# Kernel tuning notes

Measured on AMD Instinct MI355X. Metric: run time of the kernel, lower is better.

The kernel has to match this reference:

```python
import jax, jax.numpy as jnp
import numpy as np

S, B, H, I, E = 512, 2, 1024, 2816, 8  # seq_len, batch, hidden, intermediate, num_local_experts


def setup_inputs() -> dict:
    key = jax.random.key(0)
    ks = jax.random.split(key, 5)
    return {
        "hidden_states": jax.random.normal(ks[0], (S, B, H), dtype=jnp.float32),
        "router_w": jax.random.normal(ks[1], (E, H), dtype=jnp.float32) * 0.02,
        "gate_w": jax.random.normal(ks[2], (E, I, H), dtype=jnp.float32) * 0.02,
        "up_w": jax.random.normal(ks[3], (E, I, H), dtype=jnp.float32) * 0.02,
        "down_w": jax.random.normal(ks[4], (E, H, I), dtype=jnp.float32) * 0.02,
    }


def reference(hidden_states, router_w, gate_w, up_w, down_w):
    # Router: linear hidden -> num_experts, top-1 routing (num_experts_per_tok == 1).
    router_logits = jnp.einsum('sbh,eh->sbe', hidden_states, router_w)  # [S,B,E]
    routing_indices = jnp.argmax(router_logits, axis=-1)  # [S,B], top-1 == argmax
    # NOTE: the source computes routing_weights = sigmoid(top logit) but never
    # applies it in _combine_expert_outputs; we faithfully omit the scaling.

    out = jnp.zeros_like(hidden_states)
    for e in range(E):  # fixed small expert count; masked dense dispatch/combine
        mask = (routing_indices == e)[..., None]  # [S,B,1]
        xe = jnp.where(mask, hidden_states, 0.0)
        g = jnp.einsum('sbh,ih->sbi', xe, gate_w[e])
        u = jnp.einsum('sbh,ih->sbi', xe, up_w[e])
        ye = jnp.einsum('sbi,hi->sbh', jax.nn.silu(g) * u, down_w[e])
        out = out + jnp.where(mask, ye, 0.0)
    return out
```

## Files before the change

### kernel.cpp

```cpp
#include <hip/hip_runtime.h>
#include <math.h>

constexpr int H_ = 1024;
constexpr int I_ = 2816;
constexpr int E_ = 8;
constexpr int T_ = 1024;

typedef __bf16 bf16x8 __attribute__((ext_vector_type(8)));
typedef float f32x4 __attribute__((ext_vector_type(4)));

__device__ __forceinline__ ushort f2bf(float f) {
    uint32_t u = __float_as_uint(f);
    u += 0x7fff + ((u >> 16) & 1);
    return (ushort)(u >> 16);
}
__device__ __forceinline__ uint pack2(float lo, float hi) {
    return (uint)f2bf(lo) | ((uint)f2bf(hi) << 16);
}


__global__ __launch_bounds__(64) void init_counts_kernel(int* __restrict__ counts) {
    if (threadIdx.x < E_) counts[threadIdx.x] = 0;
}

__global__ __launch_bounds__(64) void router_kernel(const float* __restrict__ hidden,
                                                    const float* __restrict__ rw,
                                                    int* __restrict__ counts,
                                                    int* __restrict__ tlist) {
    const int t = blockIdx.x;
    const int lane = threadIdx.x;
    const float* x = hidden + (size_t)t * H_;
    float acc[E_];
#pragma unroll
    for (int e = 0; e < E_; e++) acc[e] = 0.f;
    for (int h = lane; h < H_; h += 64) {
        float xv = x[h];
#pragma unroll
        for (int e = 0; e < E_; e++) acc[e] = fmaf(xv, rw[e * H_ + h], acc[e]);
    }
#pragma unroll
    for (int e = 0; e < E_; e++) {
#pragma unroll
        for (int off = 32; off >= 1; off >>= 1)
            acc[e] += __shfl_xor(acc[e], off, 64);
    }
    if (lane == 0) {
        int best = 0;
        float bv = acc[0];
#pragma unroll
        for (int e = 1; e < E_; e++) {
            if (acc[e] > bv) { bv = acc[e]; best = e; }
        }
        int pos = atomicAdd(&counts[best], 1);
        tlist[best * T_ + pos] = t;
    }
}

__global__ __launch_bounds__(256) void gateup_kernel(const float* __restrict__ hidden,
                                                     const float* __restrict__ gate_w,
                                                     const float* __restrict__ up_w,
                                                     const int* __restrict__ counts,
                                                     const int* __restrict__ tlist,
                                                     ushort* __restrict__ act) {
    const int e  = blockIdx.y >> 3;
    const int tt = blockIdx.y & 7;
    const int cnt = counts[e];
    if (tt * 128 >= cnt) return;
    const int i0 = blockIdx.x * 64;
    const int tid = threadIdx.x;

    __shared__ ushort Xs[128 * 72];
    __shared__ ushort Gs[64 * 72];
    __shared__ ushort Us[64 * 72];
    __shared__ int toks[128];

    if (tid < 128) {
        int p = tt * 128 + tid;
        toks[tid] = (p < cnt) ? tlist[e * T_ + p] : -1;
    }
    __syncthreads();

    const float* gw = gate_w + (size_t)e * I_ * H_ + (size_t)i0 * H_;
    const float* uw = up_w   + (size_t)e * I_ * H_ + (size_t)i0 * H_;

    f32x4 accg[8], accu[8];
#pragma unroll
    for (int mi = 0; mi < 8; mi++) {
        accg[mi] = (f32x4){0.f, 0.f, 0.f, 0.f};
        accu[mi] = (f32x4){0.f, 0.f, 0.f, 0.f};
    }

    const int wv = tid >> 6;
    const int lane = tid & 63;
    const int quad = lane >> 4;
    const int l15 = lane & 15;

    for (int k0 = 0; k0 < H_; k0 += 64) {
        float4 xv[8];
#pragma unroll
        for (int p = 0; p < 8; p++) {
            int idx = tid + p * 256;
            int row = idx >> 4, c4 = (idx & 15) << 2;
            int tok = toks[row];
            xv[p] = (tok >= 0) ? *(const float4*)(hidden + (size_t)tok * H_ + k0 + c4)
                               : make_float4(0.f, 0.f, 0.f, 0.f);
        }
        float4 gv[4], uv[4];
#pragma unroll
        for (int p = 0; p < 4; p++) {
            int idx = tid + p * 256;
            int row = idx >> 4, c4 = (idx & 15) << 2;
            gv[p] = *(const float4*)(gw + (size_t)row * H_ + k0 + c4);
            uv[p] = *(const float4*)(uw + (size_t)row * H_ + k0 + c4);
        }
        __syncthreads();
#pragma unroll
        for (int p = 0; p < 8; p++) {
            int idx = tid + p * 256;
            int row = idx >> 4, c4 = (idx & 15) << 2;
            *(uint2*)&Xs[row * 72 + c4] = (uint2){pack2(xv[p].x, xv[p].y), pack2(xv[p].z, xv[p].w)};
        }
#pragma unroll
        for (int p = 0; p < 4; p++) {
            int idx = tid + p * 256;
            int row = idx >> 4, c4 = (idx & 15) << 2;
            *(uint2*)&Gs[row * 72 + c4] = (uint2){pack2(gv[p].x, gv[p].y), pack2(gv[p].z, gv[p].w)};
            *(uint2*)&Us[row * 72 + c4] = (uint2){pack2(uv[p].x, uv[p].y), pack2(uv[p].z, uv[p].w)};
        }
        __syncthreads();
#pragma unroll
        for (int kk = 0; kk < 64; kk += 32) {
            const int kb = kk + quad * 8;
            bf16x8 bg = *(const bf16x8*)&Gs[(wv * 16 + l15) * 72 + kb];
            bf16x8 bu = *(const bf16x8*)&Us[(wv * 16 + l15) * 72 + kb];
#pragma unroll
            for (int mi = 0; mi < 8; mi++) {
                bf16x8 a = *(const bf16x8*)&Xs[(mi * 16 + l15) * 72 + kb];
                accg[mi] = __builtin_amdgcn_mfma_f32_16x16x32_bf16(a, bg, accg[mi], 0, 0, 0);
                accu[mi] = __builtin_amdgcn_mfma_f32_16x16x32_bf16(a, bu, accu[mi], 0, 0, 0);
            }
        }
        __syncthreads();
    }

#pragma unroll
    for (int mi = 0; mi < 8; mi++) {
#pragma unroll
        for (int r = 0; r < 4; r++) {
            int tok = toks[mi * 16 + quad * 4 + r];
            if (tok < 0) continue;
            float g = accg[mi][r], u = accu[mi][r];
            float s = g / (1.f + __expf(-g)) * u;
            act[(size_t)tok * I_ + i0 + wv * 16 + l15] = f2bf(s);
        }
    }
}

__global__ __launch_bounds__(256) void down_kernel(const ushort* __restrict__ act,
                                                   const float* __restrict__ down_w,
                                                   const int* __restrict__ counts,
                                                   const int* __restrict__ tlist,
                                                   float* __restrict__ out) {
    const int e  = blockIdx.y >> 3;
    const int tt = blockIdx.y & 7;
    const int cnt = counts[e];
    if (tt * 128 >= cnt) return;
    const int h0 = blockIdx.x * 32;
    const int tid = threadIdx.x;

    __shared__ ushort As[128 * 72];
    __shared__ ushort Ds[32 * 72];
    __shared__ int toks[128];

    if (tid < 128) {
        int p = tt * 128 + tid;
        toks[tid] = (p < cnt) ? tlist[e * T_ + p] : -1;
    }
    __syncthreads();

    const float* dw = down_w + (size_t)e * H_ * I_ + (size_t)h0 * I_;

    f32x4 acc[2][2];
#pragma unroll
    for (int mi = 0; mi < 2; mi++)
#pragma unroll
        for (int nj = 0; nj < 2; nj++) acc[mi][nj] = (f32x4){0.f, 0.f, 0.f, 0.f};

    const int wv = tid >> 6;
    const int lane = tid & 63;
    const int quad = lane >> 4;
    const int l15 = lane & 15;

    for (int k0 = 0; k0 < I_; k0 += 64) {
        uint4 av[4];
#pragma unroll
        for (int p = 0; p < 4; p++) {
            int idx = tid + p * 256;
            int row = idx >> 3, c8 = (idx & 7) << 3;
            int tok = toks[row];
            av[p] = (tok >= 0) ? *(const uint4*)(act + (size_t)tok * I_ + k0 + c8)
                               : (uint4){0u, 0u, 0u, 0u};
        }
        float4 dv[2];
#pragma unroll
        for (int p = 0; p < 2; p++) {
            int idx = tid + p * 256;
            int row = idx >> 4, c4 = (idx & 15) << 2;
            dv[p] = *(const float4*)(dw + (size_t)row * I_ + k0 + c4);
        }
        __syncthreads();
#pragma unroll
        for (int p = 0; p < 4; p++) {
            int idx = tid + p * 256;
            int row = idx >> 3, c8 = (idx & 7) << 3;
            *(uint4*)&As[row * 72 + c8] = av[p];
        }
#pragma unroll
        for (int p = 0; p < 2; p++) {
            int idx = tid + p * 256;
            int row = idx >> 4, c4 = (idx & 15) << 2;
            *(uint2*)&Ds[row * 72 + c4] = (uint2){pack2(dv[p].x, dv[p].y), pack2(dv[p].z, dv[p].w)};
        }
        __syncthreads();
#pragma unroll
        for (int kk = 0; kk < 64; kk += 32) {
            const int kb = kk + quad * 8;
            bf16x8 a0 = *(const bf16x8*)&As[(wv * 32 +      l15) * 72 + kb];
            bf16x8 a1 = *(const bf16x8*)&As[(wv * 32 + 16 + l15) * 72 + kb];
            bf16x8 b0 = *(const bf16x8*)&Ds[(     l15) * 72 + kb];
            bf16x8 b1 = *(const bf16x8*)&Ds[(16 + l15) * 72 + kb];
            acc[0][0] = __builtin_amdgcn_mfma_f32_16x16x32_bf16(a0, b0, acc[0][0], 0, 0, 0);
            acc[0][1] = __builtin_amdgcn_mfma_f32_16x16x32_bf16(a0, b1, acc[0][1], 0, 0, 0);
            acc[1][0] = __builtin_amdgcn_mfma_f32_16x16x32_bf16(a1, b0, acc[1][0], 0, 0, 0);
            acc[1][1] = __builtin_amdgcn_mfma_f32_16x16x32_bf16(a1, b1, acc[1][1], 0, 0, 0);
        }
        __syncthreads();
    }

#pragma unroll
    for (int mi = 0; mi < 2; mi++) {
#pragma unroll
        for (int r = 0; r < 4; r++) {
            int tok = toks[wv * 32 + mi * 16 + quad * 4 + r];
            if (tok < 0) continue;
#pragma unroll
            for (int nj = 0; nj < 2; nj++)
                out[(size_t)tok * H_ + h0 + nj * 16 + l15] = acc[mi][nj][r];
        }
    }
}

extern "C" void kernel_launch(void* const* d_in, const int* in_sizes, int n_in,
                              void* d_out, int out_size, void* d_ws, size_t ws_size,
                              hipStream_t stream) {
    const float* hidden = (const float*)d_in[0];
    const float* rw     = (const float*)d_in[1];
    const float* gate_w = (const float*)d_in[2];
    const float* up_w   = (const float*)d_in[3];
    const float* down_w = (const float*)d_in[4];
    float* out = (float*)d_out;

    int* counts = (int*)d_ws;
    int* tlist  = counts + E_;
    ushort* act = (ushort*)(tlist + E_ * T_);

    hipLaunchKernelGGL(init_counts_kernel, dim3(1), dim3(64), 0, stream, counts);
    hipLaunchKernelGGL(router_kernel, dim3(T_), dim3(64), 0, stream, hidden, rw, counts, tlist);
    hipLaunchKernelGGL(gateup_kernel, dim3(I_ / 64, E_ * 8), dim3(256), 0, stream,
                       hidden, gate_w, up_w, counts, tlist, act);
    hipLaunchKernelGGL(down_kernel, dim3(H_ / 32, E_ * 8), dim3(256), 0, stream,
                       act, down_w, counts, tlist, out);
}
```

Before: 441.2 us.

## Stream expert weights once per block with token-loop tiles and register prefetch

The router now also writes a bf16 copy of the hidden states, so later stages gather half the bytes and skip repeated conversion. The gate/up and down kernels launch one block per (column tile, expert) and loop over that expert's tokens in chunks of 256. Each weight tile is therefore read once per expert instead of once per 128-token tile, and the next K-slice is prefetched into registers while the current one is used. This cuts the grid to fewer blocks (I/32 x 8 and H/32 x 8), which risks lower occupancy and load imbalance when experts get uneven token counts.

```diff
diff --git a/kernel.cpp b/kernel.cpp
--- a/kernel.cpp
+++ b/kernel.cpp
@@ -19,24 +19,31 @@
 }
 
 
-__global__ __launch_bounds__(64) void init_counts_kernel(int* __restrict__ counts) {
-    if (threadIdx.x < E_) counts[threadIdx.x] = 0;
-}
-
 __global__ __launch_bounds__(64) void router_kernel(const float* __restrict__ hidden,
                                                     const float* __restrict__ rw,
                                                     int* __restrict__ counts,
-                                                    int* __restrict__ tlist) {
+                                                    int* __restrict__ tlist,
+                                                    ushort* __restrict__ xbf) {
     const int t = blockIdx.x;
     const int lane = threadIdx.x;
-    const float* x = hidden + (size_t)t * H_;
+    const float* x = hidden + (size_t)t * H_ + lane * 16;
+    float4 v[4];
+#pragma unroll
+    for (int j = 0; j < 4; j++) v[j] = ((const float4*)x)[j];
+    uint2* xb = (uint2*)(xbf + (size_t)t * H_ + lane * 16);
+#pragma unroll
+    for (int j = 0; j < 4; j++) xb[j] = make_uint2(pack2(v[j].x, v[j].y), pack2(v[j].z, v[j].w));
     float acc[E_];
 #pragma unroll
-    for (int e = 0; e < E_; e++) acc[e] = 0.f;
-    for (int h = lane; h < H_; h += 64) {
-        float xv = x[h];
-#pragma unroll
-        for (int e = 0; e < E_; e++) acc[e] = fmaf(xv, rw[e * H_ + h], acc[e]);
+    for (int e = 0; e < E_; e++) {
+        const float4* r = (const float4*)(rw + e * H_ + lane * 16);
+        float a = 0.f;
+#pragma unroll
+        for (int j = 0; j < 4; j++) {
+            float4 rv = r[j];
+            a += v[j].x * rv.x + v[j].y * rv.y + v[j].z * rv.z + v[j].w * rv.w;
+        }
+        acc[e] = a;
     }
 #pragma unroll
     for (int e = 0; e < E_; e++) {
@@ -56,197 +63,241 @@
     }
 }
 
-__global__ __launch_bounds__(256) void gateup_kernel(const float* __restrict__ hidden,
-                                                     const float* __restrict__ gate_w,
-                                                     const float* __restrict__ up_w,
-                                                     const int* __restrict__ counts,
-                                                     const int* __restrict__ tlist,
-                                                     ushort* __restrict__ act) {
-    const int e  = blockIdx.y >> 3;
-    const int tt = blockIdx.y & 7;
+__global__ __launch_bounds__(256, 3) void gateup_kernel(const ushort* __restrict__ xbf,
+                                                        const float* __restrict__ gate_w,
+                                                        const float* __restrict__ up_w,
+                                                        const int* __restrict__ counts,
+                                                        const int* __restrict__ tlist,
+                                                        ushort* __restrict__ act) {
+    const int e  = blockIdx.y;
+    const int i0 = blockIdx.x * 32;
     const int cnt = counts[e];
-    if (tt * 128 >= cnt) return;
-    const int i0 = blockIdx.x * 64;
     const int tid = threadIdx.x;
 
-    __shared__ ushort Xs[128 * 72];
-    __shared__ ushort Gs[64 * 72];
-    __shared__ ushort Us[64 * 72];
-    __shared__ int toks[128];
-
-    if (tid < 128) {
-        int p = tt * 128 + tid;
-        toks[tid] = (p < cnt) ? tlist[e * T_ + p] : -1;
-    }
-    __syncthreads();
-
+    __shared__ ushort Xs[256 * 72];
+    __shared__ ushort Gs[32 * 72];
+    __shared__ ushort Us[32 * 72];
+    __shared__ int toks[256];
+
+    const int wv = tid >> 6, lane = tid & 63, quad = lane >> 4, l15 = lane & 15;
     const float* gw = gate_w + (size_t)e * I_ * H_ + (size_t)i0 * H_;
     const float* uw = up_w   + (size_t)e * I_ * H_ + (size_t)i0 * H_;
 
-    f32x4 accg[8], accu[8];
-#pragma unroll
-    for (int mi = 0; mi < 8; mi++) {
-        accg[mi] = (f32x4){0.f, 0.f, 0.f, 0.f};
-        accu[mi] = (f32x4){0.f, 0.f, 0.f, 0.f};
-    }
-
-    const int wv = tid >> 6;
-    const int lane = tid & 63;
-    const int quad = lane >> 4;
-    const int l15 = lane & 15;
-
-    for (int k0 = 0; k0 < H_; k0 += 64) {
-        float4 xv[8];
+    for (int toff = 0; toff < cnt; toff += 256) {
+        __syncthreads();
+        {
+            int p = toff + tid;
+            toks[tid] = (p < cnt) ? tlist[e * T_ + p] : -1;
+        }
+        __syncthreads();
+        int tokr[8];
+#pragma unroll
+        for (int p = 0; p < 8; p++) tokr[p] = toks[(tid + p * 256) >> 3];
+
+        f32x4 accg[4][2], accu[4][2];
+#pragma unroll
+        for (int mi = 0; mi < 4; mi++)
+#pragma unroll
+            for (int nj = 0; nj < 2; nj++) {
+                accg[mi][nj] = (f32x4){0.f, 0.f, 0.f, 0.f};
+                accu[mi][nj] = (f32x4){0.f, 0.f, 0.f, 0.f};
+            }
+
+        uint4 xv[8];
+        float4 gv[2], uv[2];
 #pragma unroll
         for (int p = 0; p < 8; p++) {
             int idx = tid + p * 256;
-            int row = idx >> 4, c4 = (idx & 15) << 2;
-            int tok = toks[row];
-            xv[p] = (tok >= 0) ? *(const float4*)(hidden + (size_t)tok * H_ + k0 + c4)
-                               : make_float4(0.f, 0.f, 0.f, 0.f);
-        }
-        float4 gv[4], uv[4];
-#pragma unroll
-        for (int p = 0; p < 4; p++) {
-            int idx = tid + p * 256;
-            int row = idx >> 4, c4 = (idx & 15) << 2;
-            gv[p] = *(const float4*)(gw + (size_t)row * H_ + k0 + c4);
-            uv[p] = *(const float4*)(uw + (size_t)row * H_ + k0 + c4);
-        }
-        __syncthreads();
-#pragma unroll
-        for (int p = 0; p < 8; p++) {
-            int idx = tid + p * 256;
-            int row = idx >> 4, c4 = (idx & 15) << 2;
-            *(uint2*)&Xs[row * 72 + c4] = (uint2){pack2(xv[p].x, xv[p].y), pack2(xv[p].z, xv[p].w)};
-        }
-#pragma unroll
-        for (int p = 0; p < 4; p++) {
-            int idx = tid + p * 256;
-            int row = idx >> 4, c4 = (idx & 15) << 2;
-            *(uint2*)&Gs[row * 72 + c4] = (uint2){pack2(gv[p].x, gv[p].y), pack2(gv[p].z, gv[p].w)};
-            *(uint2*)&Us[row * 72 + c4] = (uint2){pack2(uv[p].x, uv[p].y), pack2(uv[p].z, uv[p].w)};
-        }
-        __syncthreads();
-#pragma unroll
-        for (int kk = 0; kk < 64; kk += 32) {
-            const int kb = kk + quad * 8;
-            bf16x8 bg = *(const bf16x8*)&Gs[(wv * 16 + l15) * 72 + kb];
-            bf16x8 bu = *(const bf16x8*)&Us[(wv * 16 + l15) * 72 + kb];
-#pragma unroll
-            for (int mi = 0; mi < 8; mi++) {
-                bf16x8 a = *(const bf16x8*)&Xs[(mi * 16 + l15) * 72 + kb];
-                accg[mi] = __builtin_amdgcn_mfma_f32_16x16x32_bf16(a, bg, accg[mi], 0, 0, 0);
-                accu[mi] = __builtin_amdgcn_mfma_f32_16x16x32_bf16(a, bu, accu[mi], 0, 0, 0);
-            }
-        }
-        __syncthreads();
-    }
-
-#pragma unroll
-    for (int mi = 0; mi < 8; mi++) {
-#pragma unroll
-        for (int r = 0; r < 4; r++) {
-            int tok = toks[mi * 16 + quad * 4 + r];
-            if (tok < 0) continue;
-            float g = accg[mi][r], u = accu[mi][r];
-            float s = g / (1.f + __expf(-g)) * u;
-            act[(size_t)tok * I_ + i0 + wv * 16 + l15] = f2bf(s);
-        }
-    }
-}
-
-__global__ __launch_bounds__(256) void down_kernel(const ushort* __restrict__ act,
-                                                   const float* __restrict__ down_w,
-                                                   const int* __restrict__ counts,
-                                                   const int* __restrict__ tlist,
-                                                   float* __restrict__ out) {
-    const int e  = blockIdx.y >> 3;
-    const int tt = blockIdx.y & 7;
-    const int cnt = counts[e];
-    if (tt * 128 >= cnt) return;
-    const int h0 = blockIdx.x * 32;
-    const int tid = threadIdx.x;
-
-    __shared__ ushort As[128 * 72];
-    __shared__ ushort Ds[32 * 72];
-    __shared__ int toks[128];
-
-    if (tid < 128) {
-        int p = tt * 128 + tid;
-        toks[tid] = (p < cnt) ? tlist[e * T_ + p] : -1;
-    }
-    __syncthreads();
-
-    const float* dw = down_w + (size_t)e * H_ * I_ + (size_t)h0 * I_;
-
-    f32x4 acc[2][2];
-#pragma unroll
-    for (int mi = 0; mi < 2; mi++)
-#pragma unroll
-        for (int nj = 0; nj < 2; nj++) acc[mi][nj] = (f32x4){0.f, 0.f, 0.f, 0.f};
-
-    const int wv = tid >> 6;
-    const int lane = tid & 63;
-    const int quad = lane >> 4;
-    const int l15 = lane & 15;
-
-    for (int k0 = 0; k0 < I_; k0 += 64) {
-        uint4 av[4];
-#pragma unroll
-        for (int p = 0; p < 4; p++) {
-            int idx = tid + p * 256;
-            int row = idx >> 3, c8 = (idx & 7) << 3;
-            int tok = toks[row];
-            av[p] = (tok >= 0) ? *(const uint4*)(act + (size_t)tok * I_ + k0 + c8)
-                               : (uint4){0u, 0u, 0u, 0u};
-        }
-        float4 dv[2];
+            xv[p] = (tokr[p] >= 0)
+                ? *(const uint4*)(xbf + (size_t)tokr[p] * H_ + ((idx & 7) << 3))
+                : make_uint4(0u, 0u, 0u, 0u);
+        }
 #pragma unroll
         for (int p = 0; p < 2; p++) {
             int idx = tid + p * 256;
             int row = idx >> 4, c4 = (idx & 15) << 2;
-            dv[p] = *(const float4*)(dw + (size_t)row * I_ + k0 + c4);
-        }
+            gv[p] = *(const float4*)(gw + (size_t)row * H_ + c4);
+            uv[p] = *(const float4*)(uw + (size_t)row * H_ + c4);
+        }
+
+        for (int k0 = 0; k0 < H_; k0 += 64) {
+            __syncthreads();
+#pragma unroll
+            for (int p = 0; p < 8; p++) {
+                int idx = tid + p * 256;
+                *(uint4*)&Xs[(idx >> 3) * 72 + ((idx & 7) << 3)] = xv[p];
+            }
+#pragma unroll
+            for (int p = 0; p < 2; p++) {
+                int idx = tid + p * 256;
+                int row = idx >> 4, c4 = (idx & 15) << 2;
+                *(uint2*)&Gs[row * 72 + c4] = make_uint2(pack2(gv[p].x, gv[p].y), pack2(gv[p].z, gv[p].w));
+                *(uint2*)&Us[row * 72 + c4] = make_uint2(pack2(uv[p].x, uv[p].y), pack2(uv[p].z, uv[p].w));
+            }
+            if (k0 + 64 < H_) {
+                int kn = k0 + 64;
+#pragma unroll
+                for (int p = 0; p < 8; p++) {
+                    int idx = tid + p * 256;
+                    xv[p] = (tokr[p] >= 0)
+                        ? *(const uint4*)(xbf + (size_t)tokr[p] * H_ + kn + ((idx & 7) << 3))
+                        : make_uint4(0u, 0u, 0u, 0u);
+                }
+#pragma unroll
+                for (int p = 0; p < 2; p++) {
+                    int idx = tid + p * 256;
+                    int row = idx >> 4, c4 = (idx & 15) << 2;
+                    gv[p] = *(const float4*)(gw + (size_t)row * H_ + kn + c4);
+                    uv[p] = *(const float4*)(uw + (size_t)row * H_ + kn + c4);
+                }
+            }
+            __syncthreads();
+#pragma unroll
+            for (int kk = 0; kk < 64; kk += 32) {
+                const int kb = kk + quad * 8;
+                bf16x8 bg[2], bu[2], a[4];
+#pragma unroll
+                for (int nj = 0; nj < 2; nj++) {
+                    bg[nj] = *(const bf16x8*)&Gs[(nj * 16 + l15) * 72 + kb];
+                    bu[nj] = *(const bf16x8*)&Us[(nj * 16 + l15) * 72 + kb];
+                }
+#pragma unroll
+                for (int mi = 0; mi < 4; mi++)
+                    a[mi] = *(const bf16x8*)&Xs[(wv * 64 + mi * 16 + l15) * 72 + kb];
+#pragma unroll
+                for (int mi = 0; mi < 4; mi++)
+#pragma unroll
+                    for (int nj = 0; nj < 2; nj++) {
+                        accg[mi][nj] = __builtin_amdgcn_mfma_f32_16x16x32_bf16(a[mi], bg[nj], accg[mi][nj], 0, 0, 0);
+                        accu[mi][nj] = __builtin_amdgcn_mfma_f32_16x16x32_bf16(a[mi], bu[nj], accu[mi][nj], 0, 0, 0);
+                    }
+            }
+        }
+
+#pragma unroll
+        for (int mi = 0; mi < 4; mi++)
+#pragma unroll
+            for (int r = 0; r < 4; r++) {
+                int tok = toks[wv * 64 + mi * 16 + quad * 4 + r];
+                if (tok < 0) continue;
+#pragma unroll
+                for (int nj = 0; nj < 2; nj++) {
+                    float g = accg[mi][nj][r], u = accu[mi][nj][r];
+                    float s = g / (1.f + __expf(-g)) * u;
+                    act[(size_t)tok * I_ + i0 + nj * 16 + l15] = f2bf(s);
+                }
+            }
+    }
+}
+
+__global__ __launch_bounds__(256, 3) void down_kernel(const ushort* __restrict__ act,
+                                                      const float* __restrict__ down_w,
+                                                      const int* __restrict__ counts,
+                                                      const int* __restrict__ tlist,
+                                                      float* __restrict__ out) {
+    const int e  = blockIdx.y;
+    const int h0 = blockIdx.x * 32;
+    const int cnt = counts[e];
+    const int tid = threadIdx.x;
+
+    __shared__ ushort As[256 * 72];
+    __shared__ ushort Ds[32 * 72];
+    __shared__ int toks[256];
+
+    const int wv = tid >> 6, lane = tid & 63, quad = lane >> 4, l15 = lane & 15;
+    const float* dw = down_w + (size_t)e * H_ * I_ + (size_t)h0 * I_;
+
+    for (int toff = 0; toff < cnt; toff += 256) {
         __syncthreads();
-#pragma unroll
-        for (int p = 0; p < 4; p++) {
+        {
+            int p = toff + tid;
+            toks[tid] = (p < cnt) ? tlist[e * T_ + p] : -1;
+        }
+        __syncthreads();
+        int tokr[8];
+#pragma unroll
+        for (int p = 0; p < 8; p++) tokr[p] = toks[(tid + p * 256) >> 3];
+
+        f32x4 acc[4][2];
+#pragma unroll
+        for (int mi = 0; mi < 4; mi++)
+#pragma unroll
+            for (int nj = 0; nj < 2; nj++) acc[mi][nj] = (f32x4){0.f, 0.f, 0.f, 0.f};
+
+        uint4 av[8];
+        float4 dv[2];
+#pragma unroll
+        for (int p = 0; p < 8; p++) {
             int idx = tid + p * 256;
-            int row = idx >> 3, c8 = (idx & 7) << 3;
-            *(uint4*)&As[row * 72 + c8] = av[p];
+            av[p] = (tokr[p] >= 0)
+                ? *(const uint4*)(act + (size_t)tokr[p] * I_ + ((idx & 7) << 3))
+                : make_uint4(0u, 0u, 0u, 0u);
         }
 #pragma unroll
         for (int p = 0; p < 2; p++) {
             int idx = tid + p * 256;
             int row = idx >> 4, c4 = (idx & 15) << 2;
-            *(uint2*)&Ds[row * 72 + c4] = (uint2){pack2(dv[p].x, dv[p].y), pack2(dv[p].z, dv[p].w)};
-        }
-        __syncthreads();
-#pragma unroll
-        for (int kk = 0; kk < 64; kk += 32) {
-            const int kb = kk + quad * 8;
-            bf16x8 a0 = *(const bf16x8*)&As[(wv * 32 +      l15) * 72 + kb];
-            bf16x8 a1 = *(const bf16x8*)&As[(wv * 32 + 16 + l15) * 72 + kb];
-            bf16x8 b0 = *(const bf16x8*)&Ds[(     l15) * 72 + kb];
-            bf16x8 b1 = *(const bf16x8*)&Ds[(16 + l15) * 72 + kb];
-            acc[0][0] = __builtin_amdgcn_mfma_f32_16x16x32_bf16(a0, b0, acc[0][0], 0, 0, 0);
-            acc[0][1] = __builtin_amdgcn_mfma_f32_16x16x32_bf16(a0, b1, acc[0][1], 0, 0, 0);
-            acc[1][0] = __builtin_amdgcn_mfma_f32_16x16x32_bf16(a1, b0, acc[1][0], 0, 0, 0);
-            acc[1][1] = __builtin_amdgcn_mfma_f32_16x16x32_bf16(a1, b1, acc[1][1], 0, 0, 0);
-        }
-        __syncthreads();
-    }
-
-#pragma unroll
-    for (int mi = 0; mi < 2; mi++) {
-#pragma unroll
-        for (int r = 0; r < 4; r++) {
-            int tok = toks[wv * 32 + mi * 16 + quad * 4 + r];
-            if (tok < 0) continue;
-#pragma unroll
-            for (int nj = 0; nj < 2; nj++)
-                out[(size_t)tok * H_ + h0 + nj * 16 + l15] = acc[mi][nj][r];
-        }
+            dv[p] = *(const float4*)(dw + (size_t)row * I_ + c4);
+        }
+
+        for (int k0 = 0; k0 < I_; k0 += 64) {
+            __syncthreads();
+#pragma unroll
+            for (int p = 0; p < 8; p++) {
+                int idx = tid + p * 256;
+                *(uint4*)&As[(idx >> 3) * 72 + ((idx & 7) << 3)] = av[p];
+            }
+#pragma unroll
+            for (int p = 0; p < 2; p++) {
+                int idx = tid + p * 256;
+                int row = idx >> 4, c4 = (idx & 15) << 2;
+                *(uint2*)&Ds[row * 72 + c4] = make_uint2(pack2(dv[p].x, dv[p].y), pack2(dv[p].z, dv[p].w));
+            }
+            if (k0 + 64 < I_) {
+                int kn = k0 + 64;
+#pragma unroll
+                for (int p = 0; p < 8; p++) {
+                    int idx = tid + p * 256;
+                    av[p] = (tokr[p] >= 0)
+                        ? *(const uint4*)(act + (size_t)tokr[p] * I_ + kn + ((idx & 7) << 3))
+                        : make_uint4(0u, 0u, 0u, 0u);
+                }
+#pragma unroll
+                for (int p = 0; p < 2; p++) {
+                    int idx = tid + p * 256;
+                    int row = idx >> 4, c4 = (idx & 15) << 2;
+                    dv[p] = *(const float4*)(dw + (size_t)row * I_ + kn + c4);
+                }
+            }
+            __syncthreads();
+#pragma unroll
+            for (int kk = 0; kk < 64; kk += 32) {
+                const int kb = kk + quad * 8;
+                bf16x8 b[2], a[4];
+#pragma unroll
+                for (int nj = 0; nj < 2; nj++)
+                    b[nj] = *(const bf16x8*)&Ds[(nj * 16 + l15) * 72 + kb];
+#pragma unroll
+                for (int mi = 0; mi < 4; mi++)
+                    a[mi] = *(const bf16x8*)&As[(wv * 64 + mi * 16 + l15) * 72 + kb];
+#pragma unroll
+                for (int mi = 0; mi < 4; mi++)
+#pragma unroll
+                    for (int nj = 0; nj < 2; nj++)
+                        acc[mi][nj] = __builtin_amdgcn_mfma_f32_16x16x32_bf16(a[mi], b[nj], acc[mi][nj], 0, 0, 0);
+            }
+        }
+
+#pragma unroll
+        for (int mi = 0; mi < 4; mi++)
+#pragma unroll
+            for (int r = 0; r < 4; r++) {
+                int tok = toks[wv * 64 + mi * 16 + quad * 4 + r];
+                if (tok < 0) continue;
+#pragma unroll
+                for (int nj = 0; nj < 2; nj++)
+                    out[(size_t)tok * H_ + h0 + nj * 16 + l15] = acc[mi][nj][r];
+            }
     }
 }
 
@@ -262,12 +313,13 @@
 
     int* counts = (int*)d_ws;
     int* tlist  = counts + E_;
-    ushort* act = (ushort*)(tlist + E_ * T_);
-
-    hipLaunchKernelGGL(init_counts_kernel, dim3(1), dim3(64), 0, stream, counts);
-    hipLaunchKernelGGL(router_kernel, dim3(T_), dim3(64), 0, stream, hidden, rw, counts, tlist);
-    hipLaunchKernelGGL(gateup_kernel, dim3(I_ / 64, E_ * 8), dim3(256), 0, stream,
-                       hidden, gate_w, up_w, counts, tlist, act);
-    hipLaunchKernelGGL(down_kernel, dim3(H_ / 32, E_ * 8), dim3(256), 0, stream,
+    ushort* xbf = (ushort*)(tlist + E_ * T_);
+    ushort* act = xbf + (size_t)T_ * H_;
+
+    hipMemsetAsync(counts, 0, E_ * sizeof(int), stream);
+    hipLaunchKernelGGL(router_kernel, dim3(T_), dim3(64), 0, stream, hidden, rw, counts, tlist, xbf);
+    hipLaunchKernelGGL(gateup_kernel, dim3(I_ / 32, E_), dim3(256), 0, stream,
+                       xbf, gate_w, up_w, counts, tlist, act);
+    hipLaunchKernelGGL(down_kernel, dim3(H_ / 32, E_), dim3(256), 0, stream,
                        act, down_w, counts, tlist, out);
 }
```

New measurement: 385.3 us. -12.7%, faster.
